# Optimization experiments

Hardware: AMD Instinct MI355X
Metric: run time of the kernel (lower is better)

Reference implementation:

```python
import jax, jax.numpy as jnp
import numpy as np

L, N, D, B_, T = 4, 4, 2048, 2, 2048  # num_blocks, expansion_rate, dim, batch, seq


def setup_inputs() -> dict:
    key = jax.random.key(0)
    ks = jax.random.split(key, 12)
    f = lambda k, sh, s=0.02: s * jax.random.normal(k, sh, jnp.float32)
    x = jax.random.normal(ks[0], (B_, T, D), jnp.float32)
    # structural torch inits + small noise so grads/kernels are exercised
    eyecols = jnp.stack([jnp.eye(N, dtype=jnp.float32)[:, [i % N]] for i in range(L)])  # [L,N,1]
    A_m = eyecols + f(ks[1], (L, N, 1), 0.05)
    A_r = jnp.broadcast_to(jnp.eye(N, dtype=jnp.float32), (L, N, N)) + f(ks[2], (L, N, N), 0.05)
    Bp = jnp.ones((L, 1, N), jnp.float32) + f(ks[3], (L, 1, N), 0.05)
    W_m = f(ks[4], (L, D, 1))
    W_r = f(ks[5], (L, D, N))
    W_b = f(ks[6], (L, D, N))
    s_a = 0.01 * jnp.ones((L, 1, 1), jnp.float32)
    s_b = 0.01 * jnp.ones((L, 1, 1), jnp.float32)
    dyn_gamma = jnp.ones((L, D), jnp.float32) + f(ks[7], (L, D), 0.05)   # LayerNorm(bias=False)
    norm_gamma = jnp.ones((L, D), jnp.float32) + f(ks[8], (L, D), 0.05)  # per-block norm weight
    norm_beta = f(ks[9], (L, D))                                          # per-block norm bias
    Wblk = f(ks[10], (L, D, D), 1.0) / np.sqrt(D)                         # block = Linear(D, D)
    bblk = f(ks[11], (L, D))
    return dict(x=x, A_m=A_m, A_r=A_r, Bp=Bp, W_m=W_m, W_r=W_r, W_b=W_b,
                s_a=s_a, s_b=s_b, dyn_gamma=dyn_gamma, norm_gamma=norm_gamma,
                norm_beta=norm_beta, Wblk=Wblk, bblk=bblk)


def _ln(x, gamma, beta=None, eps=1e-5):
    mu = jnp.mean(x, axis=-1, keepdims=True)
    var = jnp.mean(jnp.square(x - mu), axis=-1, keepdims=True)
    y = (x - mu) * jax.lax.rsqrt(var + eps) * gamma
    return y if beta is None else y + beta


def reference(x, A_m, A_r, Bp, W_m, W_r, W_b, s_a, s_b,
              dyn_gamma, norm_gamma, norm_beta, Wblk, bblk):
    # hyper branch (n > 0), dynamic=True, pre_norm=True
    H = jnp.repeat(x[:, :, None, :], N, axis=2)  # [B,T,N,D]
    for i in range(L):
        # ---- width connections ----
        Hn = _ln(H, dyn_gamma[i])                                              # dynamic LN, no bias
        Am = A_m[i] + s_a[i] * jnp.tanh(jnp.einsum('btnd,do->btno', Hn, W_m[i]))  # [B,T,N,1]
        Ar = A_r[i] + s_a[i] * jnp.tanh(jnp.einsum('btnd,dm->btnm', Hn, W_r[i]))  # [B,T,N,N]
        WC = jnp.concatenate([Am, Ar], axis=-1)                                # [B,T,N,1+N]
        Ht = jnp.einsum('btnd,btnm->btdm', H, WC)                              # H^T @ WC
        h = Ht[..., 0]                                                         # [B,T,D]
        H = jnp.swapaxes(Ht[..., 1:], -2, -1)                                  # [B,T,N,D]
        # ---- pre-norm + block ----
        h = _ln(h, norm_gamma[i], norm_beta[i])
        h = jnp.einsum('btd,de->bte', h, Wblk[i]) + bblk[i]
        # ---- depth connections ----
        hn = _ln(h, dyn_gamma[i])
        Bv = Bp[i][0] + s_b[i] * jnp.tanh(jnp.einsum('btd,dn->btn', hn, W_b[i]))  # [B,T,N]
        H = H + h[:, :, None, :] * Bv[..., None]
    return H.sum(axis=2)  # [B,T,D]
```

## Files before the change

kernel.cpp:

```cpp
#include <hip/hip_runtime.h>
#include <hip/hip_bf16.h>


#define DD 2048
#define NN 4
#define LL 4
#define NTOK 4096
#define EPSF 1e-5f

typedef __attribute__((ext_vector_type(8))) short bf16x8;
typedef __attribute__((ext_vector_type(4))) float f32x4;
typedef __attribute__((ext_vector_type(2))) float f32x2;

__device__ __forceinline__ float bf2f(short u) {
  union { unsigned int i; float f; } v;
  v.i = ((unsigned int)(unsigned short)u) << 16;
  return v.f;
}
__device__ __forceinline__ short f2bf(float f) {
  __hip_bfloat16 h = __float2bfloat16(f);
  short s;
  __builtin_memcpy(&s, &h, 2);
  return s;
}
__device__ __forceinline__ float wred(float v) {
#pragma unroll
  for (int off = 32; off > 0; off >>= 1) v += __shfl_xor(v, off, 64);
  return v;
}
__device__ __forceinline__ void ld16(const void* g, void* l) {
  __builtin_amdgcn_global_load_lds(
      (const __attribute__((address_space(1))) void*)g,
      (__attribute__((address_space(3))) void*)l, 16, 0, 0);
}

__global__ __launch_bounds__(256) void prep_pack(
    const float* __restrict__ W_m, const float* __restrict__ W_r,
    const float* __restrict__ W_b, const float* __restrict__ dyn_gamma,
    const float* __restrict__ norm_gamma, const float* __restrict__ norm_beta,
    short* __restrict__ gwm, short* __restrict__ gwr, short* __restrict__ gwb,
    float* __restrict__ rb) {
  const int i = blockIdx.x * 256 + threadIdx.x;
  const float g = dyn_gamma[i];
  gwm[i] = f2bf(g * W_m[i]);
  f32x4 r = *(const f32x4*)(W_r + (size_t)i * 4);
  f32x4 b = *(const f32x4*)(W_b + (size_t)i * 4);
  short ro[4], bo[4];
#pragma unroll
  for (int k = 0; k < 4; k++) { ro[k] = f2bf(g * r[k]); bo[k] = f2bf(g * b[k]); }
  *(unsigned long long*)(gwr + (size_t)i * 4) = *(unsigned long long*)ro;
  *(unsigned long long*)(gwb + (size_t)i * 4) = *(unsigned long long*)bo;
  rb[i] = norm_beta[i] / norm_gamma[i];
}

__global__ __launch_bounds__(64) void prep_sums(
    const float* __restrict__ W_m, const float* __restrict__ W_r,
    const float* __restrict__ W_b, const float* __restrict__ dyn_gamma,
    float* __restrict__ S0w, float* __restrict__ T0d) {
  const int l = blockIdx.x;
  const int lane = threadIdx.x;
  float s[5] = {0, 0, 0, 0, 0}, t[4] = {0, 0, 0, 0};
  for (int d = lane; d < DD; d += 64) {
    const float g = dyn_gamma[l * DD + d];
    s[0] += g * W_m[l * DD + d];
    f32x4 r = *(const f32x4*)(W_r + ((size_t)l * DD + d) * 4);
    f32x4 b = *(const f32x4*)(W_b + ((size_t)l * DD + d) * 4);
#pragma unroll
    for (int m = 0; m < 4; m++) { s[1 + m] += g * r[m]; t[m] += g * b[m]; }
  }
#pragma unroll
  for (int m = 0; m < 5; m++) s[m] = wred(s[m]);
#pragma unroll
  for (int n = 0; n < 4; n++) t[n] = wred(t[n]);
  if (lane == 0) {
#pragma unroll
    for (int m = 0; m < 5; m++) S0w[l * 5 + m] = s[m];
#pragma unroll
    for (int n = 0; n < 4; n++) T0d[l * 4 + n] = t[n];
  }
}

__global__ __launch_bounds__(256) void transpose_wblk(
    const float* __restrict__ W, const float* __restrict__ norm_gamma,
    short* __restrict__ Wt) {
  __shared__ float tile[64][65];
  const int blk = blockIdx.z;
  const int c0 = blockIdx.x * 64;
  const int r0 = blockIdx.y * 64;
  const float* Ws = W + (size_t)blk * DD * DD;
  short* Wd = Wt + (size_t)blk * DD * DD;
  const int tx = threadIdx.x & 63, ty = threadIdx.x >> 6;
#pragma unroll
  for (int r = 0; r < 16; r++) {
    const int row = ty + r * 4;
    tile[row][tx] = Ws[(size_t)(r0 + row) * DD + c0 + tx];
  }
  const float gsc = norm_gamma[blk * DD + r0 + tx];
  __syncthreads();
#pragma unroll
  for (int r = 0; r < 16; r++) {
    const int row = ty + r * 4;
    Wd[(size_t)(c0 + row) * DD + r0 + tx] = f2bf(tile[tx][row] * gsc);
  }
}

__global__ __launch_bounds__(256) void row_sums(
    const short* __restrict__ Wt, const float* __restrict__ rb,
    const float* __restrict__ bblk, float* __restrict__ E0,
    float* __restrict__ E1) {
  const int l = blockIdx.y;
  const int e = blockIdx.x * 4 + (threadIdx.x >> 6);
  const int lane = threadIdx.x & 63;
  const short* row = Wt + ((size_t)l * DD + e) * DD;
  const float* rbl = rb + l * DD;
  float s1 = 0.f, s0 = 0.f;
#pragma unroll
  for (int it = 0; it < 4; it++) {
    const int d0 = lane * 8 + it * 512;
    bf16x8 w = *(const bf16x8*)(row + d0);
    f32x4 r0 = *(const f32x4*)(rbl + d0), r1 = *(const f32x4*)(rbl + d0 + 4);
#pragma unroll
    for (int q = 0; q < 8; q++) {
      const float wq = bf2f(w[q]);
      s1 += wq;
      s0 += wq * ((q < 4) ? r0[q] : r1[q - 4]);
    }
  }
  s1 = wred(s1); s0 = wred(s0);
  if (lane == 0) {
    E1[l * DD + e] = s1;
    E0[l * DD + e] = s0 + bblk[l * DD + e];
  }
}

__global__ __launch_bounds__(256) void width0_kernel(
    const float* __restrict__ x, short* __restrict__ Hst,
    short* __restrict__ hout, f32x2* __restrict__ tst,
    const float* __restrict__ A_m, const float* __restrict__ A_r,
    const short* __restrict__ gwm, const short* __restrict__ gwr,
    const float* __restrict__ s_a, const float* __restrict__ S0w) {
  const int wave = threadIdx.x >> 6;
  const int lane = threadIdx.x & 63;
  const int tok = blockIdx.x * 4 + wave;
  const int blk = 0;
  const short* wm = gwm + blk * DD;
  const short* wr = gwr + (size_t)blk * DD * 4;

  bf16x8 hreg[4];
  const float* xr = x + (size_t)tok * DD;
#pragma unroll
  for (int j = 0; j < 4; j++) {
    const int d0 = lane * 8 + j * 512;
    f32x4 a = *(const f32x4*)(xr + d0);
    f32x4 b = *(const f32x4*)(xr + d0 + 4);
    bf16x8 p;
#pragma unroll
    for (int q = 0; q < 4; q++) { p[q] = f2bf(a[q]); p[4 + q] = f2bf(b[q]); }
    hreg[j] = p;
  }

  float sH = 0, sH2 = 0, S1[5] = {0, 0, 0, 0, 0};
#pragma unroll
  for (int j = 0; j < 4; j++) {
    const int d0 = lane * 8 + j * 512;
    bf16x8 mv = *(const bf16x8*)(wm + d0);
    bf16x8 wv[4];
#pragma unroll
    for (int p = 0; p < 4; p++)
      wv[p] = *(const bf16x8*)(wr + (size_t)(d0 + 2 * p) * 4);
#pragma unroll
    for (int q = 0; q < 8; q++) {
      const float hv = bf2f(hreg[j][q]);
      sH += hv; sH2 += hv * hv;
      S1[0] += hv * bf2f(mv[q]);
#pragma unroll
      for (int m = 0; m < 4; m++)
        S1[1 + m] += hv * bf2f(wv[q >> 1][(q & 1) * 4 + m]);
    }
  }
  sH = wred(sH); sH2 = wred(sH2);
#pragma unroll
  for (int m = 0; m < 5; m++) S1[m] = wred(S1[m]);

  const float sa = s_a[blk];
  const float mu0 = sH * (1.f / DD);
  const float inv0 = rsqrtf(sH2 * (1.f / DD) - mu0 * mu0 + EPSF);
  float amSum = 0.f, arCol[NN] = {0, 0, 0, 0};
  {
    const float t0 = tanhf(inv0 * (S1[0] - mu0 * S0w[blk * 5 + 0]));
    float tm[NN];
#pragma unroll
    for (int m = 0; m < NN; m++)
      tm[m] = tanhf(inv0 * (S1[1 + m] - mu0 * S0w[blk * 5 + 1 + m]));
#pragma unroll
    for (int n = 0; n < NN; n++) {
      amSum += A_m[blk * NN + n] + sa * t0;
#pragma unroll
      for (int m = 0; m < NN; m++)
        arCol[m] += A_r[blk * NN * NN + n * NN + m] + sa * tm[m];
    }
  }

  short* Ho = Hst + (size_t)tok * NN * DD;
  short* hw = hout + (size_t)tok * DD;
  float sh = 0.f, sh2 = 0.f;
#pragma unroll
  for (int j = 0; j < 4; j++) {
    const int d0 = lane * 8 + j * 512;
    bf16x8 outp[NN], ho;
#pragma unroll
    for (int q = 0; q < 8; q++) {
      const float hv = bf2f(hreg[j][q]);
      const float a0 = hv * amSum;
      sh += a0; sh2 += a0 * a0;
      ho[q] = f2bf(a0);
#pragma unroll
      for (int m = 0; m < NN; m++) outp[m][q] = f2bf(hv * arCol[m]);
    }
    *(bf16x8*)(hw + d0) = ho;
#pragma unroll
    for (int m = 0; m < NN; m++) *(bf16x8*)(Ho + m * DD + d0) = outp[m];
  }
  sh = wred(sh); sh2 = wred(sh2);
  if (lane == 0) {
    const float mu = sh * (1.f / DD);
    const float inv = rsqrtf(sh2 * (1.f / DD) - mu * mu + EPSF);
    f32x2 t; t[0] = inv; t[1] = mu * inv;
    tst[tok] = t;
  }
}

__global__ __launch_bounds__(512) void gemm_kernel(
    const short* __restrict__ A, const short* __restrict__ Bt,
    const f32x2* __restrict__ tst, const float* __restrict__ E0,
    const float* __restrict__ E1, short* __restrict__ C) {
  __shared__ short lA[2][128 * 64];
  __shared__ short lB[2][128 * 64];
  const int tid = threadIdx.x;
  const int lane = tid & 63;
  const int wave = tid >> 6;
  const int bid = blockIdx.x;
  const int wg = (bid & 7) * 64 + (bid >> 3);
  const int m0 = (wg & 31) * 128, n0 = (wg >> 5) * 128;
  const int wm = wave >> 2;
  const int wn = wave & 3;

  f32x4 acc[4][2] = {};

#define STAGE(buf, kt)                                                        \
  {                                                                           \
    const int k0 = (kt) * 64;                                                 \
    _Pragma("unroll") for (int c = 0; c < 2; c++) {                           \
      const int idx = c * 512 + tid;                                          \
      const int row = idx >> 3;                                               \
      const int colsw = (((idx & 7) ^ (row & 7)) * 8);                        \
      ld16(A + (size_t)(m0 + row) * DD + k0 + colsw,                          \
           (char*)&lA[buf][0] + idx * 16);                                    \
      ld16(Bt + (size_t)(n0 + row) * DD + k0 + colsw,                         \
           (char*)&lB[buf][0] + idx * 16);                                    \
    }                                                                         \
  }

  STAGE(0, 0);
  __syncthreads();

  for (int kt = 0; kt < 32; ++kt) {
    const int cur = kt & 1;
    if (kt < 31) STAGE(cur ^ 1, kt + 1);
    const char* bufA = (const char*)&lA[cur][0];
    const char* bufB = (const char*)&lB[cur][0];
#pragma unroll
    for (int kk = 0; kk < 2; ++kk) {
      const int gsw = (kk * 64 + (lane >> 4) * 16) ^ ((lane & 7) << 4);
      bf16x8 af[4], bfr[2];
#pragma unroll
      for (int m = 0; m < 4; m++) {
        const int r = wm * 64 + m * 16 + (lane & 15);
        af[m] = *(const bf16x8*)(bufA + r * 128 + gsw);
      }
#pragma unroll
      for (int n = 0; n < 2; n++) {
        const int r = wn * 32 + n * 16 + (lane & 15);
        bfr[n] = *(const bf16x8*)(bufB + r * 128 + gsw);
      }
#pragma unroll
      for (int m = 0; m < 4; m++)
#pragma unroll
        for (int n = 0; n < 2; n++)
          acc[m][n] = __builtin_amdgcn_mfma_f32_16x16x32_bf16(
              af[m], bfr[n], acc[m][n], 0, 0, 0);
    }
    __syncthreads();
  }
#undef STAGE

  float e0c[2], e1c[2];
  int cols[2];
#pragma unroll
  for (int n = 0; n < 2; n++) {
    cols[n] = n0 + wn * 32 + n * 16 + (lane & 15);
    e0c[n] = E0[cols[n]];
    e1c[n] = E1[cols[n]];
  }
#pragma unroll
  for (int m = 0; m < 4; m++) {
    const int rbase = m0 + wm * 64 + m * 16 + ((lane >> 4) << 2);
#pragma unroll
    for (int j = 0; j < 4; j++) {
      const int row = rbase + j;
      const f32x2 iv = tst[row];
#pragma unroll
      for (int n = 0; n < 2; n++)
        C[(size_t)row * DD + cols[n]] =
            f2bf(iv[0] * acc[m][n][j] - iv[1] * e1c[n] + e0c[n]);
    }
  }
}

__global__ __launch_bounds__(256) void fused_dw(
    const short* __restrict__ h2, short* __restrict__ Hst,
    short* __restrict__ hout, f32x2* __restrict__ tst,
    const float* __restrict__ Bp, const short* __restrict__ gwb,
    const float* __restrict__ s_b, const float* __restrict__ A_m,
    const float* __restrict__ A_r, const short* __restrict__ gwm,
    const short* __restrict__ gwr, const float* __restrict__ s_a,
    const float* __restrict__ S0w, const float* __restrict__ T0d, int blk) {
  const int wave = threadIdx.x >> 6;
  const int lane = threadIdx.x & 63;
  const int tok = blockIdx.x * 4 + wave;
  const int nblk = blk + 1;
  const short* hr = h2 + (size_t)tok * DD;
  short* Ho = Hst + (size_t)tok * NN * DD;

  bf16x8 h2r[4];
#pragma unroll
  for (int j = 0; j < 4; j++)
    h2r[j] = *(const bf16x8*)(hr + lane * 8 + j * 512);

  const short* wb = gwb + (size_t)blk * DD * 4;
  float s1 = 0.f, s2 = 0.f, T1[NN] = {0, 0, 0, 0};
#pragma unroll
  for (int j = 0; j < 4; j++) {
    const int d0 = lane * 8 + j * 512;
    bf16x8 wv[4];
#pragma unroll
    for (int p = 0; p < 4; p++)
      wv[p] = *(const bf16x8*)(wb + (size_t)(d0 + 2 * p) * 4);
#pragma unroll
    for (int q = 0; q < 8; q++) {
      const float hv = bf2f(h2r[j][q]);
      s1 += hv; s2 += hv * hv;
#pragma unroll
      for (int n = 0; n < NN; n++)
        T1[n] += hv * bf2f(wv[q >> 1][(q & 1) * 4 + n]);
    }
  }
  s1 = wred(s1); s2 = wred(s2);
#pragma unroll
  for (int n = 0; n < NN; n++) T1[n] = wred(T1[n]);
  float Bv[NN];
  {
    const float mu = s1 * (1.f / DD);
    const float inv = rsqrtf(s2 * (1.f / DD) - mu * mu + EPSF);
    const float sb = s_b[blk];
#pragma unroll
    for (int n = 0; n < NN; n++)
      Bv[n] = Bp[blk * NN + n] +
              sb * tanhf(inv * (T1[n] - mu * T0d[blk * NN + n]));
  }

  const short* wm = gwm + nblk * DD;
  const short* wr = gwr + (size_t)nblk * DD * 4;
  float sH[NN] = {0, 0, 0, 0}, sH2[NN] = {0, 0, 0, 0};
  float S1[NN][5];
#pragma unroll
  for (int n = 0; n < NN; n++)
#pragma unroll
    for (int m = 0; m < 5; m++) S1[n][m] = 0.f;

#pragma unroll
  for (int j = 0; j < 4; j++) {
    const int d0 = lane * 8 + j * 512;
    bf16x8 hold[NN];
#pragma unroll
    for (int n = 0; n < NN; n++) hold[n] = *(const bf16x8*)(Ho + n * DD + d0);
    bf16x8 mv = *(const bf16x8*)(wm + d0);
    bf16x8 wv[4];
#pragma unroll
    for (int p = 0; p < 4; p++)
      wv[p] = *(const bf16x8*)(wr + (size_t)(d0 + 2 * p) * 4);
#pragma unroll
    for (int q = 0; q < 8; q++) {
      const float hv2 = bf2f(h2r[j][q]);
      float gw[5];
      gw[0] = bf2f(mv[q]);
#pragma unroll
      for (int m = 0; m < 4; m++)
        gw[1 + m] = bf2f(wv[q >> 1][(q & 1) * 4 + m]);
#pragma unroll
      for (int n = 0; n < NN; n++) {
        const float hp = bf2f(hold[n][q]) + hv2 * Bv[n];
        sH[n] += hp; sH2[n] += hp * hp;
#pragma unroll
        for (int m = 0; m < 5; m++) S1[n][m] += hp * gw[m];
      }
    }
  }
#pragma unroll
  for (int n = 0; n < NN; n++) { sH[n] = wred(sH[n]); sH2[n] = wred(sH2[n]); }
#pragma unroll
  for (int n = 0; n < NN; n++)
#pragma unroll
    for (int m = 0; m < 5; m++) S1[n][m] = wred(S1[n][m]);

  const float sa = s_a[nblk];
  float Am[NN], Ar[NN][NN];
#pragma unroll
  for (int n = 0; n < NN; n++) {
    const float mu = sH[n] * (1.f / DD);
    const float var = sH2[n] * (1.f / DD) - mu * mu;
    const float inv = rsqrtf(var + EPSF);
    Am[n] = A_m[nblk * NN + n] +
            sa * tanhf(inv * (S1[n][0] - mu * S0w[nblk * 5 + 0]));
#pragma unroll
    for (int m = 0; m < NN; m++)
      Ar[n][m] = A_r[nblk * NN * NN + n * NN + m] +
                 sa * tanhf(inv * (S1[n][1 + m] - mu * S0w[nblk * 5 + 1 + m]));
  }

  short* hw = hout + (size_t)tok * DD;
  float sh = 0.f, sh2 = 0.f;
#pragma unroll
  for (int j = 0; j < 4; j++) {
    const int d0 = lane * 8 + j * 512;
    bf16x8 hold[NN];
#pragma unroll
    for (int n = 0; n < NN; n++) hold[n] = *(const bf16x8*)(Ho + n * DD + d0);
    bf16x8 outp[NN], ho;
#pragma unroll
    for (int q = 0; q < 8; q++) {
      const float hv2 = bf2f(h2r[j][q]);
      float hp[NN];
#pragma unroll
      for (int n = 0; n < NN; n++) hp[n] = bf2f(hold[n][q]) + hv2 * Bv[n];
      float a0 = 0.f, am0 = 0.f, am1 = 0.f, am2 = 0.f, am3 = 0.f;
#pragma unroll
      for (int n = 0; n < NN; n++) {
        a0 += hp[n] * Am[n];
        am0 += hp[n] * Ar[n][0];
        am1 += hp[n] * Ar[n][1];
        am2 += hp[n] * Ar[n][2];
        am3 += hp[n] * Ar[n][3];
      }
      sh += a0; sh2 += a0 * a0;
      ho[q] = f2bf(a0);
      outp[0][q] = f2bf(am0); outp[1][q] = f2bf(am1);
      outp[2][q] = f2bf(am2); outp[3][q] = f2bf(am3);
    }
    *(bf16x8*)(hw + d0) = ho;
#pragma unroll
    for (int m = 0; m < NN; m++) *(bf16x8*)(Ho + m * DD + d0) = outp[m];
  }
  sh = wred(sh); sh2 = wred(sh2);
  if (lane == 0) {
    const float mu = sh * (1.f / DD);
    const float inv = rsqrtf(sh2 * (1.f / DD) - mu * mu + EPSF);
    f32x2 t; t[0] = inv; t[1] = mu * inv;
    tst[tok] = t;
  }
}

__global__ __launch_bounds__(256) void depth_last(
    const short* __restrict__ h2, const short* __restrict__ Hst,
    float* __restrict__ out, const float* __restrict__ Bp,
    const short* __restrict__ gwb, const float* __restrict__ s_b,
    const float* __restrict__ T0d, int blk) {
  const int wave = threadIdx.x >> 6;
  const int lane = threadIdx.x & 63;
  const int tok = blockIdx.x * 4 + wave;
  const short* hr = h2 + (size_t)tok * DD;
  const short* wb = gwb + (size_t)blk * DD * 4;

  bf16x8 h2r[4];
  float s1 = 0.f, s2 = 0.f, T1[NN] = {0, 0, 0, 0};
#pragma unroll
  for (int j = 0; j < 4; j++) {
    const int d0 = lane * 8 + j * 512;
    h2r[j] = *(const bf16x8*)(hr + d0);
    bf16x8 wv[4];
#pragma unroll
    for (int p = 0; p < 4; p++)
      wv[p] = *(const bf16x8*)(wb + (size_t)(d0 + 2 * p) * 4);
#pragma unroll
    for (int q = 0; q < 8; q++) {
      const float hv = bf2f(h2r[j][q]);
      s1 += hv; s2 += hv * hv;
#pragma unroll
      for (int n = 0; n < NN; n++)
        T1[n] += hv * bf2f(wv[q >> 1][(q & 1) * 4 + n]);
    }
  }
  s1 = wred(s1); s2 = wred(s2);
#pragma unroll
  for (int n = 0; n < NN; n++) T1[n] = wred(T1[n]);
  const float mu = s1 * (1.f / DD);
  const float inv = rsqrtf(s2 * (1.f / DD) - mu * mu + EPSF);
  const float sb = s_b[blk];
  float bsum = 0.f;
#pragma unroll
  for (int n = 0; n < NN; n++)
    bsum += Bp[blk * NN + n] + sb * tanhf(inv * (T1[n] - mu * T0d[blk * NN + n]));

  const short* Ho = Hst + (size_t)tok * NN * DD;
  float* orow = out + (size_t)tok * DD;
#pragma unroll
  for (int j = 0; j < 4; j++) {
    const int d0 = lane * 8 + j * 512;
    bf16x8 hrow[NN];
#pragma unroll
    for (int n = 0; n < NN; n++) hrow[n] = *(const bf16x8*)(Ho + n * DD + d0);
    f32x4 o0, o1;
#pragma unroll
    for (int q = 0; q < 8; q++) {
      const float hv = bf2f(h2r[j][q]);
      float s = hv * bsum;
#pragma unroll
      for (int n = 0; n < NN; n++) s += bf2f(hrow[n][q]);
      if (q < 4) o0[q] = s; else o1[q - 4] = s;
    }
    *(f32x4*)(orow + d0) = o0;
    *(f32x4*)(orow + d0 + 4) = o1;
  }
}

extern "C" void kernel_launch(void* const* d_in, const int* in_sizes, int n_in,
                              void* d_out, int out_size, void* d_ws,
                              size_t ws_size, hipStream_t stream) {
  const float* x = (const float*)d_in[0];
  const float* A_m = (const float*)d_in[1];
  const float* A_r = (const float*)d_in[2];
  const float* Bp = (const float*)d_in[3];
  const float* W_m = (const float*)d_in[4];
  const float* W_r = (const float*)d_in[5];
  const float* W_b = (const float*)d_in[6];
  const float* s_a = (const float*)d_in[7];
  const float* s_b = (const float*)d_in[8];
  const float* dyn_gamma = (const float*)d_in[9];
  const float* norm_gamma = (const float*)d_in[10];
  const float* norm_beta = (const float*)d_in[11];
  const float* Wblk = (const float*)d_in[12];
  const float* bblk = (const float*)d_in[13];
  float* out = (float*)d_out;

  char* ws = (char*)d_ws;
  short* Hst = (short*)(ws);
  short* hbuf = (short*)(ws + 67108864);
  short* h2 = (short*)(ws + 83886080);
  char* aux = ws + 100663296;
  short* gwm = (short*)(aux);
  short* gwr = (short*)(aux + 16384);
  short* gwb = (short*)(aux + 16384 + 65536);
  float* rb = (float*)(aux + 16384 + 131072);
  float* S0w = (float*)(aux + 16384 + 131072 + 32768);
  float* T0d = (float*)(aux + 16384 + 131072 + 32768 + 128);
  f32x2* tst = (f32x2*)(aux + 16384 + 131072 + 32768 + 256);
  float* E0 = (float*)(aux + 16384 + 131072 + 32768 + 256 + 32768);
  float* E1 = E0 + LL * DD;
  short* Wt = (short*)d_out;

  dim3 tb(256);
  prep_pack<<<32, tb, 0, stream>>>(W_m, W_r, W_b, dyn_gamma, norm_gamma,
                                   norm_beta, gwm, gwr, gwb, rb);
  prep_sums<<<4, dim3(64), 0, stream>>>(W_m, W_r, W_b, dyn_gamma, S0w, T0d);
  transpose_wblk<<<dim3(32, 32, 4), tb, 0, stream>>>(Wblk, norm_gamma, Wt);
  row_sums<<<dim3(512, 4), tb, 0, stream>>>(Wt, rb, bblk, E0, E1);
  width0_kernel<<<1024, tb, 0, stream>>>(x, Hst, hbuf, tst, A_m, A_r, gwm,
                                         gwr, s_a, S0w);
  for (int i = 0; i < LL; i++) {
    gemm_kernel<<<512, dim3(512), 0, stream>>>(
        hbuf, Wt + (size_t)i * DD * DD, tst, E0 + i * DD, E1 + i * DD, h2);
    if (i < LL - 1)
      fused_dw<<<1024, tb, 0, stream>>>(h2, Hst, hbuf, tst, Bp, gwb, s_b, A_m,
                                        A_r, gwm, gwr, s_a, S0w, T0d, i);
    else
      depth_last<<<1024, tb, 0, stream>>>(h2, Hst, out, Bp, gwb, s_b, T0d, i);
  }
}
```

Measured before the change: 369.1 us.

## Represent hyper-streams as coefficient combos of basis vectors with Gram-matrix statistics

Instead of materializing the 4-stream H tensor per token, each stream is kept as a small coefficient vector over basis rows (the input x and each block output h2). LayerNorm statistics and the width projections are computed algebraically from stored sums, Gram entries and per-basis projections. The kernels therefore read and write basis rows plus a few scalars rather than the full 4xD state. This removes most of the H-state memory traffic, at the cost of keeping all block outputs alive and reading a growing number of basis rows per step. Computing variance from Gram sums may also lose some numerical precision.

```diff
diff --git a/kernel.cpp b/kernel.cpp
--- a/kernel.cpp
+++ b/kernel.cpp
@@ -7,6 +7,7 @@
 #define LL 4
 #define NTOK 4096
 #define EPSF 1e-5f
+#define STS 80
 
 typedef __attribute__((ext_vector_type(8))) short bf16x8;
 typedef __attribute__((ext_vector_type(4))) float f32x4;
@@ -32,6 +33,12 @@
   __builtin_amdgcn_global_load_lds(
       (const __attribute__((address_space(1))) void*)g,
       (__attribute__((address_space(3))) void*)l, 16, 0, 0);
+}
+__host__ __device__ constexpr int pofs(int k, int l) {
+  return k == 0 ? 20 + l * 5
+       : k == 1 ? 40 + (l - 1) * 5
+       : k == 2 ? 55 + (l - 2) * 5
+                : 65;
 }
 
 __global__ __launch_bounds__(256) void prep_pack(
@@ -134,20 +141,19 @@
 }
 
 __global__ __launch_bounds__(256) void width0_kernel(
-    const float* __restrict__ x, short* __restrict__ Hst,
-    short* __restrict__ hout, f32x2* __restrict__ tst,
-    const float* __restrict__ A_m, const float* __restrict__ A_r,
-    const short* __restrict__ gwm, const short* __restrict__ gwr,
-    const float* __restrict__ s_a, const float* __restrict__ S0w) {
+    const float* __restrict__ x, short* __restrict__ b0,
+    short* __restrict__ hout, f32x2* __restrict__ tst, float* __restrict__ Cc,
+    float* __restrict__ ST, const float* __restrict__ A_m,
+    const float* __restrict__ A_r, const short* __restrict__ gwm,
+    const short* __restrict__ gwr, const float* __restrict__ s_a,
+    const float* __restrict__ S0w) {
   const int wave = threadIdx.x >> 6;
   const int lane = threadIdx.x & 63;
   const int tok = blockIdx.x * 4 + wave;
-  const int blk = 0;
-  const short* wm = gwm + blk * DD;
-  const short* wr = gwr + (size_t)blk * DD * 4;
-
-  bf16x8 hreg[4];
   const float* xr = x + (size_t)tok * DD;
+  short* b0t = b0 + (size_t)tok * DD;
+
+  bf16x8 xb[4];
 #pragma unroll
   for (int j = 0; j < 4; j++) {
     const int d0 = lane * 8 + j * 512;
@@ -156,77 +162,89 @@
     bf16x8 p;
 #pragma unroll
     for (int q = 0; q < 4; q++) { p[q] = f2bf(a[q]); p[4 + q] = f2bf(b[q]); }
-    hreg[j] = p;
-  }
-
-  float sH = 0, sH2 = 0, S1[5] = {0, 0, 0, 0, 0};
+    xb[j] = p;
+    *(bf16x8*)(b0t + d0) = p;
+  }
+
+  float o = 0.f, qq = 0.f, P0[4][5];
+#pragma unroll
+  for (int l = 0; l < 4; l++)
+#pragma unroll
+    for (int m = 0; m < 5; m++) P0[l][m] = 0.f;
+
 #pragma unroll
   for (int j = 0; j < 4; j++) {
     const int d0 = lane * 8 + j * 512;
-    bf16x8 mv = *(const bf16x8*)(wm + d0);
-    bf16x8 wv[4];
-#pragma unroll
-    for (int p = 0; p < 4; p++)
-      wv[p] = *(const bf16x8*)(wr + (size_t)(d0 + 2 * p) * 4);
+    bf16x8 wmv[4], wrv[4][4];
+#pragma unroll
+    for (int l = 0; l < 4; l++) {
+      wmv[l] = *(const bf16x8*)(gwm + l * DD + d0);
+#pragma unroll
+      for (int p = 0; p < 4; p++)
+        wrv[l][p] = *(const bf16x8*)(gwr + ((size_t)l * DD + d0 + 2 * p) * 4);
+    }
 #pragma unroll
     for (int q = 0; q < 8; q++) {
-      const float hv = bf2f(hreg[j][q]);
-      sH += hv; sH2 += hv * hv;
-      S1[0] += hv * bf2f(mv[q]);
-#pragma unroll
-      for (int m = 0; m < 4; m++)
-        S1[1 + m] += hv * bf2f(wv[q >> 1][(q & 1) * 4 + m]);
-    }
-  }
-  sH = wred(sH); sH2 = wred(sH2);
-#pragma unroll
-  for (int m = 0; m < 5; m++) S1[m] = wred(S1[m]);
-
-  const float sa = s_a[blk];
-  const float mu0 = sH * (1.f / DD);
-  const float inv0 = rsqrtf(sH2 * (1.f / DD) - mu0 * mu0 + EPSF);
-  float amSum = 0.f, arCol[NN] = {0, 0, 0, 0};
-  {
-    const float t0 = tanhf(inv0 * (S1[0] - mu0 * S0w[blk * 5 + 0]));
-    float tm[NN];
-#pragma unroll
-    for (int m = 0; m < NN; m++)
-      tm[m] = tanhf(inv0 * (S1[1 + m] - mu0 * S0w[blk * 5 + 1 + m]));
-#pragma unroll
-    for (int n = 0; n < NN; n++) {
-      amSum += A_m[blk * NN + n] + sa * t0;
-#pragma unroll
-      for (int m = 0; m < NN; m++)
-        arCol[m] += A_r[blk * NN * NN + n * NN + m] + sa * tm[m];
-    }
-  }
-
-  short* Ho = Hst + (size_t)tok * NN * DD;
+      const float hv = bf2f(xb[j][q]);
+      o += hv; qq += hv * hv;
+#pragma unroll
+      for (int l = 0; l < 4; l++) {
+        P0[l][0] += hv * bf2f(wmv[l][q]);
+#pragma unroll
+        for (int m = 0; m < 4; m++)
+          P0[l][1 + m] += hv * bf2f(wrv[l][q >> 1][(q & 1) * 4 + m]);
+      }
+    }
+  }
+  o = wred(o); qq = wred(qq);
+#pragma unroll
+  for (int l = 0; l < 4; l++)
+#pragma unroll
+    for (int m = 0; m < 5; m++) P0[l][m] = wred(P0[l][m]);
+
+  const float sa = s_a[0];
+  const float mu = o * (1.f / DD);
+  const float inv = rsqrtf(qq * (1.f / DD) - mu * mu + EPSF);
+  const float t0 = tanhf(inv * (P0[0][0] - mu * S0w[0]));
+  float tm[4];
+#pragma unroll
+  for (int m = 0; m < 4; m++)
+    tm[m] = tanhf(inv * (P0[0][1 + m] - mu * S0w[1 + m]));
+  float amSum = 0.f, arCol[4] = {0, 0, 0, 0};
+#pragma unroll
+  for (int n = 0; n < 4; n++) {
+    amSum += A_m[n] + sa * t0;
+#pragma unroll
+    for (int m = 0; m < 4; m++) arCol[m] += A_r[n * 4 + m] + sa * tm[m];
+  }
+
+  if (lane == 0) {
+    const float sh = amSum * o;
+    const float sh2 = amSum * amSum * qq;
+    const float mu2 = sh * (1.f / DD);
+    const float inv2 = rsqrtf(sh2 * (1.f / DD) - mu2 * mu2 + EPSF);
+    f32x2 t; t[0] = inv2; t[1] = mu2 * inv2;
+    tst[tok] = t;
+    float* STt = ST + (size_t)tok * STS;
+    STt[0] = o;
+    STt[4] = qq;
+#pragma unroll
+    for (int l = 0; l < 4; l++)
+#pragma unroll
+      for (int m = 0; m < 5; m++) STt[pofs(0, l) + m] = P0[l][m];
+    float* Ct = Cc + (size_t)tok * 16;
+#pragma unroll
+    for (int n = 0; n < 4; n++) Ct[n * 4] = arCol[n];
+  }
+
   short* hw = hout + (size_t)tok * DD;
-  float sh = 0.f, sh2 = 0.f;
 #pragma unroll
   for (int j = 0; j < 4; j++) {
     const int d0 = lane * 8 + j * 512;
-    bf16x8 outp[NN], ho;
-#pragma unroll
-    for (int q = 0; q < 8; q++) {
-      const float hv = bf2f(hreg[j][q]);
-      const float a0 = hv * amSum;
-      sh += a0; sh2 += a0 * a0;
-      ho[q] = f2bf(a0);
-#pragma unroll
-      for (int m = 0; m < NN; m++) outp[m][q] = f2bf(hv * arCol[m]);
-    }
+    bf16x8 ho;
+#pragma unroll
+    for (int q = 0; q < 8; q++) ho[q] = f2bf(amSum * bf2f(xb[j][q]));
     *(bf16x8*)(hw + d0) = ho;
-#pragma unroll
-    for (int m = 0; m < NN; m++) *(bf16x8*)(Ho + m * DD + d0) = outp[m];
-  }
-  sh = wred(sh); sh2 = wred(sh2);
-  if (lane == 0) {
-    const float mu = sh * (1.f / DD);
-    const float inv = rsqrtf(sh2 * (1.f / DD) - mu * mu + EPSF);
-    f32x2 t; t[0] = inv; t[1] = mu * inv;
-    tst[tok] = t;
   }
 }
 
@@ -317,215 +335,287 @@
   }
 }
 
+template <int I>
 __global__ __launch_bounds__(256) void fused_dw(
-    const short* __restrict__ h2, short* __restrict__ Hst,
-    short* __restrict__ hout, f32x2* __restrict__ tst,
-    const float* __restrict__ Bp, const short* __restrict__ gwb,
+    const short* __restrict__ h2s, const short* __restrict__ b0,
+    short* __restrict__ hout, f32x2* __restrict__ tst, float* __restrict__ Cc,
+    float* __restrict__ ST, const float* __restrict__ Bp,
     const float* __restrict__ s_b, const float* __restrict__ A_m,
-    const float* __restrict__ A_r, const short* __restrict__ gwm,
-    const short* __restrict__ gwr, const float* __restrict__ s_a,
-    const float* __restrict__ S0w, const float* __restrict__ T0d, int blk) {
+    const float* __restrict__ A_r, const float* __restrict__ s_a,
+    const float* __restrict__ S0w, const float* __restrict__ T0d,
+    const short* __restrict__ gwm, const short* __restrict__ gwr,
+    const short* __restrict__ gwb) {
+  constexpr int NB = I + 1;
+  constexpr int NP = 3 - I;
   const int wave = threadIdx.x >> 6;
   const int lane = threadIdx.x & 63;
   const int tok = blockIdx.x * 4 + wave;
-  const int nblk = blk + 1;
-  const short* hr = h2 + (size_t)tok * DD;
-  short* Ho = Hst + (size_t)tok * NN * DD;
+
+  const short* vt = h2s + ((size_t)I * NTOK + tok) * DD;
+  const short* bases[I + 1];
+  bases[0] = b0 + (size_t)tok * DD;
+#pragma unroll
+  for (int k = 1; k <= I; k++)
+    bases[k] = h2s + ((size_t)(k - 1) * NTOK + tok) * DD;
 
   bf16x8 h2r[4];
 #pragma unroll
   for (int j = 0; j < 4; j++)
-    h2r[j] = *(const bf16x8*)(hr + lane * 8 + j * 512);
-
-  const short* wb = gwb + (size_t)blk * DD * 4;
-  float s1 = 0.f, s2 = 0.f, T1[NN] = {0, 0, 0, 0};
+    h2r[j] = *(const bf16x8*)(vt + lane * 8 + j * 512);
+
+  float o = 0.f;
+  float Gr[I + 2] = {};
+  float Tb[4] = {0, 0, 0, 0};
+  float Pn[NP][5];
+#pragma unroll
+  for (int li = 0; li < NP; li++)
+#pragma unroll
+    for (int m = 0; m < 5; m++) Pn[li][m] = 0.f;
+
 #pragma unroll
   for (int j = 0; j < 4; j++) {
     const int d0 = lane * 8 + j * 512;
-    bf16x8 wv[4];
+    bf16x8 bsv[I + 1];
+#pragma unroll
+    for (int k = 0; k <= I; k++) bsv[k] = *(const bf16x8*)(bases[k] + d0);
+    bf16x8 wbv[4];
 #pragma unroll
     for (int p = 0; p < 4; p++)
-      wv[p] = *(const bf16x8*)(wb + (size_t)(d0 + 2 * p) * 4);
+      wbv[p] = *(const bf16x8*)(gwb + ((size_t)I * DD + d0 + 2 * p) * 4);
+    bf16x8 wmv[NP], wrv[NP][4];
+#pragma unroll
+    for (int li = 0; li < NP; li++) {
+      const int l = NB + li;
+      wmv[li] = *(const bf16x8*)(gwm + l * DD + d0);
+#pragma unroll
+      for (int p = 0; p < 4; p++)
+        wrv[li][p] = *(const bf16x8*)(gwr + ((size_t)l * DD + d0 + 2 * p) * 4);
+    }
 #pragma unroll
     for (int q = 0; q < 8; q++) {
       const float hv = bf2f(h2r[j][q]);
-      s1 += hv; s2 += hv * hv;
-#pragma unroll
-      for (int n = 0; n < NN; n++)
-        T1[n] += hv * bf2f(wv[q >> 1][(q & 1) * 4 + n]);
-    }
-  }
-  s1 = wred(s1); s2 = wred(s2);
-#pragma unroll
-  for (int n = 0; n < NN; n++) T1[n] = wred(T1[n]);
-  float Bv[NN];
+      o += hv;
+      Gr[I + 1] += hv * hv;
+#pragma unroll
+      for (int k = 0; k <= I; k++) Gr[k] += hv * bf2f(bsv[k][q]);
+#pragma unroll
+      for (int n = 0; n < 4; n++)
+        Tb[n] += hv * bf2f(wbv[q >> 1][(q & 1) * 4 + n]);
+#pragma unroll
+      for (int li = 0; li < NP; li++) {
+        Pn[li][0] += hv * bf2f(wmv[li][q]);
+#pragma unroll
+        for (int m = 0; m < 4; m++)
+          Pn[li][1 + m] += hv * bf2f(wrv[li][q >> 1][(q & 1) * 4 + m]);
+      }
+    }
+  }
+  o = wred(o);
+#pragma unroll
+  for (int k = 0; k <= I + 1; k++) Gr[k] = wred(Gr[k]);
+#pragma unroll
+  for (int n = 0; n < 4; n++) Tb[n] = wred(Tb[n]);
+#pragma unroll
+  for (int li = 0; li < NP; li++)
+#pragma unroll
+    for (int m = 0; m < 5; m++) Pn[li][m] = wred(Pn[li][m]);
+
+  float* STt = ST + (size_t)tok * STS;
+  float* Ct = Cc + (size_t)tok * 16;
+  float ofull[I + 2], Gf[I + 2][I + 2], Pf[I + 2][5], Cp[4][I + 2];
+#pragma unroll
+  for (int k = 0; k <= I; k++) ofull[k] = STt[k];
+  ofull[I + 1] = o;
+#pragma unroll
+  for (int k = 0; k <= I; k++)
+#pragma unroll
+    for (int j2 = 0; j2 <= I; j2++) Gf[k][j2] = STt[4 + k * 4 + j2];
+#pragma unroll
+  for (int k = 0; k <= I; k++) { Gf[k][I + 1] = Gr[k]; Gf[I + 1][k] = Gr[k]; }
+  Gf[I + 1][I + 1] = Gr[I + 1];
+#pragma unroll
+  for (int k = 0; k <= I; k++)
+#pragma unroll
+    for (int m = 0; m < 5; m++) Pf[k][m] = STt[pofs(k, NB) + m];
+#pragma unroll
+  for (int m = 0; m < 5; m++) Pf[I + 1][m] = Pn[0][m];
+#pragma unroll
+  for (int n = 0; n < 4; n++)
+#pragma unroll
+    for (int k = 0; k <= I; k++) Cp[n][k] = Ct[n * 4 + k];
+
   {
-    const float mu = s1 * (1.f / DD);
-    const float inv = rsqrtf(s2 * (1.f / DD) - mu * mu + EPSF);
-    const float sb = s_b[blk];
-#pragma unroll
-    for (int n = 0; n < NN; n++)
-      Bv[n] = Bp[blk * NN + n] +
-              sb * tanhf(inv * (T1[n] - mu * T0d[blk * NN + n]));
-  }
-
-  const short* wm = gwm + nblk * DD;
-  const short* wr = gwr + (size_t)nblk * DD * 4;
-  float sH[NN] = {0, 0, 0, 0}, sH2[NN] = {0, 0, 0, 0};
-  float S1[NN][5];
-#pragma unroll
-  for (int n = 0; n < NN; n++)
-#pragma unroll
-    for (int m = 0; m < 5; m++) S1[n][m] = 0.f;
-
-#pragma unroll
-  for (int j = 0; j < 4; j++) {
-    const int d0 = lane * 8 + j * 512;
-    bf16x8 hold[NN];
-#pragma unroll
-    for (int n = 0; n < NN; n++) hold[n] = *(const bf16x8*)(Ho + n * DD + d0);
-    bf16x8 mv = *(const bf16x8*)(wm + d0);
-    bf16x8 wv[4];
-#pragma unroll
-    for (int p = 0; p < 4; p++)
-      wv[p] = *(const bf16x8*)(wr + (size_t)(d0 + 2 * p) * 4);
-#pragma unroll
-    for (int q = 0; q < 8; q++) {
-      const float hv2 = bf2f(h2r[j][q]);
-      float gw[5];
-      gw[0] = bf2f(mv[q]);
-#pragma unroll
-      for (int m = 0; m < 4; m++)
-        gw[1 + m] = bf2f(wv[q >> 1][(q & 1) * 4 + m]);
-#pragma unroll
-      for (int n = 0; n < NN; n++) {
-        const float hp = bf2f(hold[n][q]) + hv2 * Bv[n];
-        sH[n] += hp; sH2[n] += hp * hp;
-#pragma unroll
-        for (int m = 0; m < 5; m++) S1[n][m] += hp * gw[m];
-      }
-    }
-  }
-#pragma unroll
-  for (int n = 0; n < NN; n++) { sH[n] = wred(sH[n]); sH2[n] = wred(sH2[n]); }
-#pragma unroll
-  for (int n = 0; n < NN; n++)
-#pragma unroll
-    for (int m = 0; m < 5; m++) S1[n][m] = wred(S1[n][m]);
-
-  const float sa = s_a[nblk];
-  float Am[NN], Ar[NN][NN];
-#pragma unroll
-  for (int n = 0; n < NN; n++) {
-    const float mu = sH[n] * (1.f / DD);
-    const float var = sH2[n] * (1.f / DD) - mu * mu;
-    const float inv = rsqrtf(var + EPSF);
-    Am[n] = A_m[nblk * NN + n] +
-            sa * tanhf(inv * (S1[n][0] - mu * S0w[nblk * 5 + 0]));
-#pragma unroll
-    for (int m = 0; m < NN; m++)
-      Ar[n][m] = A_r[nblk * NN * NN + n * NN + m] +
-                 sa * tanhf(inv * (S1[n][1 + m] - mu * S0w[nblk * 5 + 1 + m]));
-  }
-
-  short* hw = hout + (size_t)tok * DD;
-  float sh = 0.f, sh2 = 0.f;
-#pragma unroll
-  for (int j = 0; j < 4; j++) {
-    const int d0 = lane * 8 + j * 512;
-    bf16x8 hold[NN];
-#pragma unroll
-    for (int n = 0; n < NN; n++) hold[n] = *(const bf16x8*)(Ho + n * DD + d0);
-    bf16x8 outp[NN], ho;
-#pragma unroll
-    for (int q = 0; q < 8; q++) {
-      const float hv2 = bf2f(h2r[j][q]);
-      float hp[NN];
-#pragma unroll
-      for (int n = 0; n < NN; n++) hp[n] = bf2f(hold[n][q]) + hv2 * Bv[n];
-      float a0 = 0.f, am0 = 0.f, am1 = 0.f, am2 = 0.f, am3 = 0.f;
-#pragma unroll
-      for (int n = 0; n < NN; n++) {
-        a0 += hp[n] * Am[n];
-        am0 += hp[n] * Ar[n][0];
-        am1 += hp[n] * Ar[n][1];
-        am2 += hp[n] * Ar[n][2];
-        am3 += hp[n] * Ar[n][3];
-      }
-      sh += a0; sh2 += a0 * a0;
-      ho[q] = f2bf(a0);
-      outp[0][q] = f2bf(am0); outp[1][q] = f2bf(am1);
-      outp[2][q] = f2bf(am2); outp[3][q] = f2bf(am3);
-    }
-    *(bf16x8*)(hw + d0) = ho;
-#pragma unroll
-    for (int m = 0; m < NN; m++) *(bf16x8*)(Ho + m * DD + d0) = outp[m];
-  }
-  sh = wred(sh); sh2 = wred(sh2);
+    const float mu2 = o * (1.f / DD);
+    const float inv2 = rsqrtf(Gr[I + 1] * (1.f / DD) - mu2 * mu2 + EPSF);
+    const float sb = s_b[I];
+#pragma unroll
+    for (int n = 0; n < 4; n++)
+      Cp[n][I + 1] = Bp[I * 4 + n] +
+                     sb * tanhf(inv2 * (Tb[n] - mu2 * T0d[I * 4 + n]));
+  }
+
+  const float sa = s_a[NB];
+  float Am[4], Ar[4][4];
+#pragma unroll
+  for (int n = 0; n < 4; n++) {
+    float sH = 0.f, sH2 = 0.f;
+#pragma unroll
+    for (int k = 0; k <= I + 1; k++) {
+      sH += Cp[n][k] * ofull[k];
+#pragma unroll
+      for (int j2 = 0; j2 <= I + 1; j2++)
+        sH2 += Cp[n][k] * Cp[n][j2] * Gf[k][j2];
+    }
+    const float mu = sH * (1.f / DD);
+    const float inv = rsqrtf(sH2 * (1.f / DD) - mu * mu + EPSF);
+    float S1[5];
+#pragma unroll
+    for (int m = 0; m < 5; m++) {
+      S1[m] = 0.f;
+#pragma unroll
+      for (int k = 0; k <= I + 1; k++) S1[m] += Cp[n][k] * Pf[k][m];
+    }
+    Am[n] = A_m[NB * 4 + n] +
+            sa * tanhf(inv * (S1[0] - mu * S0w[NB * 5 + 0]));
+#pragma unroll
+    for (int m = 0; m < 4; m++)
+      Ar[n][m] = A_r[NB * 16 + n * 4 + m] +
+                 sa * tanhf(inv * (S1[1 + m] - mu * S0w[NB * 5 + 1 + m]));
+  }
+
+  float Cn[4][I + 2], hc[I + 2];
+#pragma unroll
+  for (int k = 0; k <= I + 1; k++) {
+    hc[k] = 0.f;
+#pragma unroll
+    for (int n = 0; n < 4; n++) hc[k] += Am[n] * Cp[n][k];
+  }
+#pragma unroll
+  for (int mr = 0; mr < 4; mr++)
+#pragma unroll
+    for (int k = 0; k <= I + 1; k++) {
+      float acc = 0.f;
+#pragma unroll
+      for (int n = 0; n < 4; n++) acc += Ar[n][mr] * Cp[n][k];
+      Cn[mr][k] = acc;
+    }
+
   if (lane == 0) {
+    float sh = 0.f, sh2 = 0.f;
+#pragma unroll
+    for (int k = 0; k <= I + 1; k++) {
+      sh += hc[k] * ofull[k];
+#pragma unroll
+      for (int j2 = 0; j2 <= I + 1; j2++) sh2 += hc[k] * hc[j2] * Gf[k][j2];
+    }
     const float mu = sh * (1.f / DD);
     const float inv = rsqrtf(sh2 * (1.f / DD) - mu * mu + EPSF);
     f32x2 t; t[0] = inv; t[1] = mu * inv;
     tst[tok] = t;
+    STt[I + 1] = o;
+#pragma unroll
+    for (int k = 0; k <= I + 1; k++) {
+      STt[4 + (I + 1) * 4 + k] = Gf[I + 1][k];
+      STt[4 + k * 4 + (I + 1)] = Gf[k][I + 1];
+    }
+#pragma unroll
+    for (int li = 1; li < NP; li++)
+#pragma unroll
+      for (int m = 0; m < 5; m++) STt[pofs(I + 1, NB + li) + m] = Pn[li][m];
+#pragma unroll
+    for (int n = 0; n < 4; n++)
+#pragma unroll
+      for (int k = 0; k <= I + 1; k++) Ct[n * 4 + k] = Cn[n][k];
+  }
+
+  short* hw = hout + (size_t)tok * DD;
+#pragma unroll
+  for (int j = 0; j < 4; j++) {
+    const int d0 = lane * 8 + j * 512;
+    bf16x8 bsv[I + 1];
+#pragma unroll
+    for (int k = 0; k <= I; k++) bsv[k] = *(const bf16x8*)(bases[k] + d0);
+    bf16x8 ho;
+#pragma unroll
+    for (int q = 0; q < 8; q++) {
+      float a = hc[I + 1] * bf2f(h2r[j][q]);
+#pragma unroll
+      for (int k = 0; k <= I; k++) a += hc[k] * bf2f(bsv[k][q]);
+      ho[q] = f2bf(a);
+    }
+    *(bf16x8*)(hw + d0) = ho;
   }
 }
 
 __global__ __launch_bounds__(256) void depth_last(
-    const short* __restrict__ h2, const short* __restrict__ Hst,
-    float* __restrict__ out, const float* __restrict__ Bp,
-    const short* __restrict__ gwb, const float* __restrict__ s_b,
-    const float* __restrict__ T0d, int blk) {
+    const short* __restrict__ h2s, const short* __restrict__ b0,
+    float* __restrict__ out, const float* __restrict__ Cc,
+    const float* __restrict__ Bp, const float* __restrict__ s_b,
+    const float* __restrict__ T0d, const short* __restrict__ gwb) {
   const int wave = threadIdx.x >> 6;
   const int lane = threadIdx.x & 63;
   const int tok = blockIdx.x * 4 + wave;
-  const short* hr = h2 + (size_t)tok * DD;
-  const short* wb = gwb + (size_t)blk * DD * 4;
+  const short* vt = h2s + ((size_t)3 * NTOK + tok) * DD;
 
   bf16x8 h2r[4];
-  float s1 = 0.f, s2 = 0.f, T1[NN] = {0, 0, 0, 0};
+  float s1 = 0.f, s2 = 0.f, Tb[4] = {0, 0, 0, 0};
 #pragma unroll
   for (int j = 0; j < 4; j++) {
     const int d0 = lane * 8 + j * 512;
-    h2r[j] = *(const bf16x8*)(hr + d0);
-    bf16x8 wv[4];
+    h2r[j] = *(const bf16x8*)(vt + d0);
+    bf16x8 wbv[4];
 #pragma unroll
     for (int p = 0; p < 4; p++)
-      wv[p] = *(const bf16x8*)(wb + (size_t)(d0 + 2 * p) * 4);
+      wbv[p] = *(const bf16x8*)(gwb + ((size_t)3 * DD + d0 + 2 * p) * 4);
 #pragma unroll
     for (int q = 0; q < 8; q++) {
       const float hv = bf2f(h2r[j][q]);
       s1 += hv; s2 += hv * hv;
 #pragma unroll
-      for (int n = 0; n < NN; n++)
-        T1[n] += hv * bf2f(wv[q >> 1][(q & 1) * 4 + n]);
+      for (int n = 0; n < 4; n++)
+        Tb[n] += hv * bf2f(wbv[q >> 1][(q & 1) * 4 + n]);
     }
   }
   s1 = wred(s1); s2 = wred(s2);
 #pragma unroll
-  for (int n = 0; n < NN; n++) T1[n] = wred(T1[n]);
+  for (int n = 0; n < 4; n++) Tb[n] = wred(Tb[n]);
+
   const float mu = s1 * (1.f / DD);
   const float inv = rsqrtf(s2 * (1.f / DD) - mu * mu + EPSF);
-  const float sb = s_b[blk];
+  const float sb = s_b[3];
   float bsum = 0.f;
 #pragma unroll
-  for (int n = 0; n < NN; n++)
-    bsum += Bp[blk * NN + n] + sb * tanhf(inv * (T1[n] - mu * T0d[blk * NN + n]));
-
-  const short* Ho = Hst + (size_t)tok * NN * DD;
+  for (int n = 0; n < 4; n++)
+    bsum += Bp[12 + n] + sb * tanhf(inv * (Tb[n] - mu * T0d[12 + n]));
+
+  const float* Ct = Cc + (size_t)tok * 16;
+  float e[4];
+#pragma unroll
+  for (int k = 0; k < 4; k++) {
+    e[k] = 0.f;
+#pragma unroll
+    for (int n = 0; n < 4; n++) e[k] += Ct[n * 4 + k];
+  }
+
+  const short* bases[4];
+  bases[0] = b0 + (size_t)tok * DD;
+#pragma unroll
+  for (int k = 1; k < 4; k++)
+    bases[k] = h2s + ((size_t)(k - 1) * NTOK + tok) * DD;
+
   float* orow = out + (size_t)tok * DD;
 #pragma unroll
   for (int j = 0; j < 4; j++) {
     const int d0 = lane * 8 + j * 512;
-    bf16x8 hrow[NN];
-#pragma unroll
-    for (int n = 0; n < NN; n++) hrow[n] = *(const bf16x8*)(Ho + n * DD + d0);
+    bf16x8 bsv[4];
+#pragma unroll
+    for (int k = 0; k < 4; k++) bsv[k] = *(const bf16x8*)(bases[k] + d0);
     f32x4 o0, o1;
 #pragma unroll
     for (int q = 0; q < 8; q++) {
-      const float hv = bf2f(h2r[j][q]);
-      float s = hv * bsum;
-#pragma unroll
-      for (int n = 0; n < NN; n++) s += bf2f(hrow[n][q]);
+      float s = bsum * bf2f(h2r[j][q]);
+#pragma unroll
+      for (int k = 0; k < 4; k++) s += e[k] * bf2f(bsv[k][q]);
       if (q < 4) o0[q] = s; else o1[q - 4] = s;
     }
     *(f32x4*)(orow + d0) = o0;
@@ -553,19 +643,21 @@
   float* out = (float*)d_out;
 
   char* ws = (char*)d_ws;
-  short* Hst = (short*)(ws);
-  short* hbuf = (short*)(ws + 67108864);
-  short* h2 = (short*)(ws + 83886080);
+  short* b0 = (short*)(ws);
+  short* h2s = (short*)(ws + 16777216);
+  short* hnorm = (short*)(ws + 83886080);
   char* aux = ws + 100663296;
   short* gwm = (short*)(aux);
   short* gwr = (short*)(aux + 16384);
-  short* gwb = (short*)(aux + 16384 + 65536);
-  float* rb = (float*)(aux + 16384 + 131072);
-  float* S0w = (float*)(aux + 16384 + 131072 + 32768);
-  float* T0d = (float*)(aux + 16384 + 131072 + 32768 + 128);
-  f32x2* tst = (f32x2*)(aux + 16384 + 131072 + 32768 + 256);
-  float* E0 = (float*)(aux + 16384 + 131072 + 32768 + 256 + 32768);
-  float* E1 = E0 + LL * DD;
+  short* gwb = (short*)(aux + 81920);
+  float* rb = (float*)(aux + 147456);
+  float* S0w = (float*)(aux + 180224);
+  float* T0d = (float*)(aux + 181248);
+  f32x2* tst = (f32x2*)(aux + 182272);
+  float* E0 = (float*)(aux + 215040);
+  float* E1 = (float*)(aux + 247808);
+  float* Cc = (float*)(aux + 280576);
+  float* ST = (float*)(aux + 542720);
   short* Wt = (short*)d_out;
 
   dim3 tb(256);
@@ -574,15 +666,25 @@
   prep_sums<<<4, dim3(64), 0, stream>>>(W_m, W_r, W_b, dyn_gamma, S0w, T0d);
   transpose_wblk<<<dim3(32, 32, 4), tb, 0, stream>>>(Wblk, norm_gamma, Wt);
   row_sums<<<dim3(512, 4), tb, 0, stream>>>(Wt, rb, bblk, E0, E1);
-  width0_kernel<<<1024, tb, 0, stream>>>(x, Hst, hbuf, tst, A_m, A_r, gwm,
-                                         gwr, s_a, S0w);
+  width0_kernel<<<1024, tb, 0, stream>>>(x, b0, hnorm, tst, Cc, ST, A_m, A_r,
+                                         gwm, gwr, s_a, S0w);
   for (int i = 0; i < LL; i++) {
     gemm_kernel<<<512, dim3(512), 0, stream>>>(
-        hbuf, Wt + (size_t)i * DD * DD, tst, E0 + i * DD, E1 + i * DD, h2);
-    if (i < LL - 1)
-      fused_dw<<<1024, tb, 0, stream>>>(h2, Hst, hbuf, tst, Bp, gwb, s_b, A_m,
-                                        A_r, gwm, gwr, s_a, S0w, T0d, i);
+        hnorm, Wt + (size_t)i * DD * DD, tst, E0 + i * DD, E1 + i * DD,
+        h2s + (size_t)i * NTOK * DD);
+    if (i == 0)
+      fused_dw<0><<<1024, tb, 0, stream>>>(h2s, b0, hnorm, tst, Cc, ST, Bp,
+                                           s_b, A_m, A_r, s_a, S0w, T0d, gwm,
+                                           gwr, gwb);
+    else if (i == 1)
+      fused_dw<1><<<1024, tb, 0, stream>>>(h2s, b0, hnorm, tst, Cc, ST, Bp,
+                                           s_b, A_m, A_r, s_a, S0w, T0d, gwm,
+                                           gwr, gwb);
+    else if (i == 2)
+      fused_dw<2><<<1024, tb, 0, stream>>>(h2s, b0, hnorm, tst, Cc, ST, Bp,
+                                           s_b, A_m, A_r, s_a, S0w, T0d, gwm,
+                                           gwr, gwb);
     else
-      depth_last<<<1024, tb, 0, stream>>>(h2, Hst, out, Bp, gwb, s_b, T0d, i);
-  }
-}
+      depth_last<<<1024, tb, 0, stream>>>(h2s, b0, out, Cc, Bp, s_b, T0d, gwb);
+  }
+}
```

Result: faster. 326.7 us (-11.5%).
